# Performance work log

Measured on AMD Instinct MI355X. Metric: run time of the kernel, lower is better.

## Reference

```python
import jax, jax.numpy as jnp
import numpy as np

NUM_CLASSES = 10  # matches label fill_max; original iterates over train_label.unique()


def setup_inputs() -> dict:
    key = jax.random.key(0)
    k1, k2, k3 = jax.random.split(key, 3)
    n, m, d = 8192, 50000, 128
    x = jax.random.normal(k1, (n, d), dtype=jnp.float32)
    train_pts = jax.random.normal(k2, (m, d), dtype=jnp.float32)
    train_label = jax.random.randint(k3, (m,), 0, NUM_CLASSES, dtype=jnp.int32)
    return {"x": x, "train_pts": train_pts, "train_label": train_label, "k": 10}


def reference(x, train_pts, train_label, k):
    # Euclidean distance matrix [n, m]; same math as expand/pow/sum without the
    x2 = jnp.sum(x * x, axis=1, keepdims=True)          # [n, 1]
    y2 = jnp.sum(train_pts * train_pts, axis=1)         # [m]
    sq = x2 + y2[None, :] - 2.0 * (x @ train_pts.T)     # [n, m]
    dist = jnp.sqrt(jnp.maximum(sq, 0.0))
    # k smallest distances -> neighbor indices
    _, idx = jax.lax.top_k(-dist, k)                    # [n, k]
    votes = train_label[idx]                            # [n, k]
    # per-class vote counts; original loop: for lab in sorted unique labels,
    # who = count >= best -> ties go to the LARGEST label
    counts = jnp.sum(jax.nn.one_hot(votes, NUM_CLASSES, dtype=jnp.int32), axis=1)  # [n, C]
    winner = (NUM_CLASSES - 1) - jnp.argmax(counts[:, ::-1], axis=1)
    return winner.astype(train_label.dtype)
```

## Files before the change

### kernel.cpp

```cpp
#include <hip/hip_runtime.h>
#include <float.h>
#include <limits.h>

#define N_Q 8192
#define M_PTS 50000
#define DIM 128
#define KNN 10
#define NCLS 10
#define NCHUNK 16
#define TPC 196
#define CPC 8
#define NCAND (NCHUNK*CPC)
#define NSEL 24
#define TPL 6
#define QPB 128
#define SBIAS 256.0f
#define YTHREADS 200000
#define PTHREADS 232768
#define ATHREADS 232944

typedef __attribute__((ext_vector_type(8))) int i32x8;
typedef __attribute__((ext_vector_type(4))) float f32x4;
typedef unsigned int u32;

__device__ __forceinline__ u32 pack4_e4m3(float4 v, float sc) {
    u32 w = 0;
    w = __builtin_amdgcn_cvt_pk_fp8_f32(sc * v.x, sc * v.y, w, false);
    w = __builtin_amdgcn_cvt_pk_fp8_f32(sc * v.z, sc * v.w, w, true);
    return w;
}

__global__ __launch_bounds__(256) void prep_kernel(
    const float4* __restrict__ x4, const float4* __restrict__ y4,
    u32* __restrict__ xb8, u32* __restrict__ yt8, float* __restrict__ y2) {
    int t = blockIdx.x * 256 + threadIdx.x;
    if (t < YTHREADS) {
        int T = t >> 6, l = t & 63, nr = l & 15, g = l >> 4;
        const float4* src = y4 + ((size_t)(T * 16 + nr) * DIM + g * 32) / 4;
        u32 w[8];
        float ss = 0.f;
        #pragma unroll
        for (int i = 0; i < 8; ++i) {
            float4 v = src[i];
            ss += v.x * v.x + v.y * v.y + v.z * v.z + v.w * v.w;
            w[i] = pack4_e4m3(v, 1.0f);
        }
        uint4* dst = (uint4*)(yt8 + (size_t)T * 512 + l * 8);
        dst[0] = make_uint4(w[0], w[1], w[2], w[3]);
        dst[1] = make_uint4(w[4], w[5], w[6], w[7]);
        ss += __shfl_xor(ss, 16, 64);
        ss += __shfl_xor(ss, 32, 64);
        if (l < 16) y2[T * 16 + l] = ss + SBIAS;
    } else if (t < PTHREADS) {
        int tx = t - YTHREADS, row = tx >> 2, g = tx & 3;
        const float4* src = x4 + ((size_t)row * DIM + g * 32) / 4;
        u32 w[8];
        #pragma unroll
        for (int i = 0; i < 8; ++i) w[i] = pack4_e4m3(src[i], -2.0f);
        uint4* dst = (uint4*)(xb8 + (size_t)row * 32 + g * 8);
        dst[0] = make_uint4(w[0], w[1], w[2], w[3]);
        dst[1] = make_uint4(w[4], w[5], w[6], w[7]);
    } else if (t < ATHREADS) {
        y2[M_PTS + (t - PTHREADS)] = FLT_MAX;
    }
}

__global__ __launch_bounds__(256, 4) void knn_filter(
    const u32* __restrict__ xb8, const u32* __restrict__ yt8,
    const float* __restrict__ y2, u32* __restrict__ ckey) {
    const int lane = threadIdx.x & 63;
    const int wid  = threadIdx.x >> 6;
    const int g    = lane >> 4;
    const int nrow = lane & 15;
    const int chunk = blockIdx.x;
    const int qb    = blockIdx.y;
    const int qw = qb * QPB + wid * 32;

    i32x8 bq0 = *(const i32x8*)(xb8 + (size_t)(qw + nrow) * 32 + g * 8);
    i32x8 bq1 = *(const i32x8*)(xb8 + (size_t)(qw + 16 + nrow) * 32 + g * 8);

    float ts0[TPL], ts1[TPL];
    #pragma unroll
    for (int l = 0; l < TPL; ++l) { ts0[l] = FLT_MAX; ts1[l] = FLT_MAX; }

    const u32* ytp = yt8 + (size_t)chunk * TPC * 512 + lane * 8;
    const f32x4* y2p = (const f32x4*)(y2 + chunk * TPC * 16 + g * 4);

    #pragma unroll 2
    for (int t = 0; t < TPC; ++t) {
        i32x8 ay = *(const i32x8*)(ytp + (size_t)t * 512);
        f32x4 cq = y2p[t * 4];
        f32x4 d0 = __builtin_amdgcn_mfma_scale_f32_16x16x128_f8f6f4(
            ay, bq0, cq, 0, 0, 0, 0x7F7F7F7F, 0, 0x7F7F7F7F);
        f32x4 d1 = __builtin_amdgcn_mfma_scale_f32_16x16x128_f8f6f4(
            ay, bq1, cq, 0, 0, 0, 0x7F7F7F7F, 0, 0x7F7F7F7F);
        u32 relb = (u32)(t * 16) | (u32)(g * 4);
        #pragma unroll
        for (int i = 0; i < 4; ++i) {
            float k0 = __uint_as_float((__float_as_uint(d0[i]) & 0xFFFFF000u) | (relb + i));
            float k1 = __uint_as_float((__float_as_uint(d1[i]) & 0xFFFFF000u) | (relb + i));
            float a0 = ts0[0], a1 = ts0[1], a2 = ts0[2], a3 = ts0[3], a4 = ts0[4];
            float b0 = ts1[0], b1 = ts1[1], b2 = ts1[2], b3 = ts1[3], b4 = ts1[4];
            ts0[0] = fminf(a0, k0);
            ts1[0] = fminf(b0, k1);
            ts0[1] = __builtin_amdgcn_fmed3f(k0, a0, a1);
            ts1[1] = __builtin_amdgcn_fmed3f(k1, b0, b1);
            ts0[2] = __builtin_amdgcn_fmed3f(k0, a1, a2);
            ts1[2] = __builtin_amdgcn_fmed3f(k1, b1, b2);
            ts0[3] = __builtin_amdgcn_fmed3f(k0, a2, a3);
            ts1[3] = __builtin_amdgcn_fmed3f(k1, b2, b3);
            ts0[4] = __builtin_amdgcn_fmed3f(k0, a3, a4);
            ts1[4] = __builtin_amdgcn_fmed3f(k1, b3, b4);
            ts0[5] = __builtin_amdgcn_fmed3f(k0, a4, ts0[5]);
            ts1[5] = __builtin_amdgcn_fmed3f(k1, b4, ts1[5]);
        }
    }

    __shared__ u32 smem[QPB * 25];
    {
        int ql0 = wid * 32 + nrow;
        int ql1 = wid * 32 + 16 + nrow;
        #pragma unroll
        for (int l = 0; l < TPL; ++l) {
            smem[ql0 * 25 + g * TPL + l] = __float_as_uint(ts0[l]);
            smem[ql1 * 25 + g * TPL + l] = __float_as_uint(ts1[l]);
        }
    }
    __syncthreads();
    if (threadIdx.x < QPB) {
        int ql = threadIdx.x;
        float bs[CPC];
        #pragma unroll
        for (int i = 0; i < CPC; ++i) bs[i] = FLT_MAX;
        for (int e = 0; e < 4 * TPL; ++e) {
            float f = __uint_as_float(smem[ql * 25 + e]);
            #pragma unroll
            for (int q2 = 0; q2 < CPC; ++q2) {
                float mn = fminf(bs[q2], f);
                f = fmaxf(bs[q2], f);
                bs[q2] = mn;
            }
        }
        u32* dst = ckey + ((size_t)(qb * QPB + ql) * NCHUNK + chunk) * CPC;
        #pragma unroll
        for (int i = 0; i < CPC; ++i) dst[i] = __float_as_uint(bs[i]);
    }
}

__global__ __launch_bounds__(256) void knn_finalize(
    const u32* __restrict__ ckey, const float* __restrict__ x,
    const float* __restrict__ y, const int* __restrict__ labels,
    int* __restrict__ out) {
    const int lane = threadIdx.x & 63;
    const int wid  = threadIdx.x >> 6;
    const int qbase = blockIdx.x * 8;
    const int ql = wid * 2 + (lane >> 5);
    const int sl = lane & 31;

    __shared__ u32 skey[8][NCAND];
    __shared__ int sidx[8][NSEL];
    __shared__ double sex[8][NSEL];

    for (int i = threadIdx.x; i < 8 * NCAND; i += 256)
        skey[i >> 7][i & 127] = ckey[(size_t)(qbase + (i >> 7)) * NCAND + (i & 127)];
    __syncthreads();

    {
        u32 ke[4];
        int rank[4];
        #pragma unroll
        for (int r0 = 0; r0 < 4; ++r0) {
            ke[r0] = skey[ql][r0 * 32 + sl];
            rank[r0] = 0;
        }
        for (int j = 0; j < NCAND; ++j) {
            u32 kj = skey[ql][j];
            #pragma unroll
            for (int r0 = 0; r0 < 4; ++r0)
                rank[r0] += (kj < ke[r0] || (kj == ke[r0] && j < r0 * 32 + sl)) ? 1 : 0;
        }
        #pragma unroll
        for (int r0 = 0; r0 < 4; ++r0) {
            if (rank[r0] < NSEL) {
                int e = r0 * 32 + sl;
                sidx[ql][rank[r0]] = (e >> 3) * (TPC * 16) + (int)(ke[r0] & 0xFFFu);
            }
        }
    }
    __syncthreads();

    if (sl < NSEL) {
        const int idx = sidx[ql][sl];
        const float4* xr = (const float4*)(x + (size_t)(qbase + ql) * DIM);
        const float4* yr = (const float4*)(y + (size_t)idx * DIM);
        double dy2 = 0.0, dxy = 0.0;
        #pragma unroll 8
        for (int i = 0; i < 32; ++i) {
            float4 yv = yr[i];
            float4 xv = xr[i];
            dy2 = fma((double)yv.x, (double)yv.x, dy2);
            dy2 = fma((double)yv.y, (double)yv.y, dy2);
            dy2 = fma((double)yv.z, (double)yv.z, dy2);
            dy2 = fma((double)yv.w, (double)yv.w, dy2);
            dxy = fma((double)xv.x, (double)yv.x, dxy);
            dxy = fma((double)xv.y, (double)yv.y, dxy);
            dxy = fma((double)xv.z, (double)yv.z, dxy);
            dxy = fma((double)xv.w, (double)yv.w, dxy);
        }
        sex[ql][sl] = dy2 - 2.0 * dxy;
    }
    __syncthreads();

    if (sl == 0) {
        double tsv[KNN]; int ti[KNN];
        #pragma unroll
        for (int i = 0; i < KNN; ++i) { tsv[i] = 1e300; ti[i] = INT_MAX; }
        #pragma unroll
        for (int c = 0; c < NSEL; ++c) {
            double s = sex[ql][c];
            int id = sidx[ql][c];
            #pragma unroll
            for (int pp = 0; pp < KNN; ++pp) {
                bool lt = (s < tsv[pp]) || (s == tsv[pp] && id < ti[pp]);
                double ns = lt ? tsv[pp] : s;  int nid = lt ? ti[pp] : id;
                tsv[pp] = lt ? s : tsv[pp];    ti[pp] = lt ? id : ti[pp];
                s = ns; id = nid;
            }
        }
        int lab[KNN];
        #pragma unroll
        for (int i = 0; i < KNN; ++i) lab[i] = labels[ti[i]];
        int bestc = 0, bestn = -1;
        #pragma unroll
        for (int c = 0; c < NCLS; ++c) {
            int n = 0;
            #pragma unroll
            for (int i = 0; i < KNN; ++i) n += (lab[i] == c) ? 1 : 0;
            if (n >= bestn) { bestn = n; bestc = c; }
        }
        out[qbase + ql] = bestc;
    }
}

extern "C" void kernel_launch(void* const* d_in, const int* in_sizes, int n_in,
                              void* d_out, int out_size, void* d_ws, size_t ws_size,
                              hipStream_t stream) {
    const float* x      = (const float*)d_in[0];
    const float* y      = (const float*)d_in[1];
    const int*   labels = (const int*)d_in[2];

    char* ws = (char*)d_ws;
    size_t off = 0;
    u32* xb8 = (u32*)(ws + off);    off += (size_t)N_Q * DIM;
    u32* yt8 = (u32*)(ws + off);    off += (size_t)NCHUNK * TPC * 2048;
    float* y2 = (float*)(ws + off); off += (size_t)NCHUNK * TPC * 16 * 4;
    u32* ckey = (u32*)(ws + off);   off += (size_t)N_Q * NCAND * 4;
    int* out = (int*)d_out;

    prep_kernel<<<(ATHREADS + 255) / 256, 256, 0, stream>>>(
        (const float4*)x, (const float4*)y, xb8, yt8, y2);
    knn_filter<<<dim3(NCHUNK, N_Q / QPB), 256, 0, stream>>>(xb8, yt8, y2, ckey);
    knn_finalize<<<N_Q / 8, 256, 0, stream>>>(ckey, x, y, labels, out);
}
```

Measured before the change: 274.0 us.

## Prefetch tiles in filter loop and coalesce prep with one float4 per thread

The filter kernel's main loop now loads the next pair of FP8 tiles and their norm vectors before running the MFMA and top-k updates on the current pair. This is register double-buffering meant to hide global load latency behind compute. The prep kernel is rewritten so each thread converts one float4, which makes the fp32 reads coalesced. Row norms are then reduced with a 32-lane shuffle tree, at the cost of scattered 4-byte stores into the tiled layout. The prefetch also raises register pressure under launch bounds of (256,4).

```diff
diff --git a/kernel.cpp b/kernel.cpp
--- a/kernel.cpp
+++ b/kernel.cpp
@@ -15,9 +15,8 @@
 #define TPL 6
 #define QPB 128
 #define SBIAS 256.0f
-#define YTHREADS 200000
-#define PTHREADS 232768
-#define ATHREADS 232944
+#define XN4 (N_Q*DIM/4)
+#define YN4 (M_PTS*DIM/4)
 
 typedef __attribute__((ext_vector_type(8))) int i32x8;
 typedef __attribute__((ext_vector_type(4))) float f32x4;
@@ -34,34 +33,23 @@
     const float4* __restrict__ x4, const float4* __restrict__ y4,
     u32* __restrict__ xb8, u32* __restrict__ yt8, float* __restrict__ y2) {
     int t = blockIdx.x * 256 + threadIdx.x;
-    if (t < YTHREADS) {
-        int T = t >> 6, l = t & 63, nr = l & 15, g = l >> 4;
-        const float4* src = y4 + ((size_t)(T * 16 + nr) * DIM + g * 32) / 4;
-        u32 w[8];
-        float ss = 0.f;
-        #pragma unroll
-        for (int i = 0; i < 8; ++i) {
-            float4 v = src[i];
-            ss += v.x * v.x + v.y * v.y + v.z * v.z + v.w * v.w;
-            w[i] = pack4_e4m3(v, 1.0f);
-        }
-        uint4* dst = (uint4*)(yt8 + (size_t)T * 512 + l * 8);
-        dst[0] = make_uint4(w[0], w[1], w[2], w[3]);
-        dst[1] = make_uint4(w[4], w[5], w[6], w[7]);
-        ss += __shfl_xor(ss, 16, 64);
-        ss += __shfl_xor(ss, 32, 64);
-        if (l < 16) y2[T * 16 + l] = ss + SBIAS;
-    } else if (t < PTHREADS) {
-        int tx = t - YTHREADS, row = tx >> 2, g = tx & 3;
-        const float4* src = x4 + ((size_t)row * DIM + g * 32) / 4;
-        u32 w[8];
-        #pragma unroll
-        for (int i = 0; i < 8; ++i) w[i] = pack4_e4m3(src[i], -2.0f);
-        uint4* dst = (uint4*)(xb8 + (size_t)row * 32 + g * 8);
-        dst[0] = make_uint4(w[0], w[1], w[2], w[3]);
-        dst[1] = make_uint4(w[4], w[5], w[6], w[7]);
-    } else if (t < ATHREADS) {
-        y2[M_PTS + (t - PTHREADS)] = FLT_MAX;
+    if (t < XN4) {
+        xb8[t] = pack4_e4m3(x4[t], -2.0f);
+    } else if (t < XN4 + YN4) {
+        int j = t - XN4;
+        int row = j >> 5;
+        int d4  = j & 31;
+        float4 v = y4[j];
+        u32 w = pack4_e4m3(v, 1.0f);
+        int T = row >> 4, nr = row & 15;
+        int g2 = d4 >> 3, s = d4 & 7;
+        yt8[(size_t)T * 512 + (g2 * 16 + nr) * 8 + s] = w;
+        float p = v.x * v.x + v.y * v.y + v.z * v.z + v.w * v.w;
+        #pragma unroll
+        for (int off = 16; off > 0; off >>= 1) p += __shfl_xor(p, off, 64);
+        if (d4 == 0) y2[row] = p + SBIAS;
+    } else if (t < XN4 + YN4 + 176) {
+        y2[M_PTS + (t - XN4 - YN4)] = FLT_MAX;
     }
 }
 
@@ -86,10 +74,7 @@
     const u32* ytp = yt8 + (size_t)chunk * TPC * 512 + lane * 8;
     const f32x4* y2p = (const f32x4*)(y2 + chunk * TPC * 16 + g * 4);
 
-    #pragma unroll 2
-    for (int t = 0; t < TPC; ++t) {
-        i32x8 ay = *(const i32x8*)(ytp + (size_t)t * 512);
-        f32x4 cq = y2p[t * 4];
+    auto process = [&](i32x8 ay, f32x4 cq, int t) {
         f32x4 d0 = __builtin_amdgcn_mfma_scale_f32_16x16x128_f8f6f4(
             ay, bq0, cq, 0, 0, 0, 0x7F7F7F7F, 0, 0x7F7F7F7F);
         f32x4 d1 = __builtin_amdgcn_mfma_scale_f32_16x16x128_f8f6f4(
@@ -114,7 +99,26 @@
             ts0[5] = __builtin_amdgcn_fmed3f(k0, a4, ts0[5]);
             ts1[5] = __builtin_amdgcn_fmed3f(k1, b4, ts1[5]);
         }
-    }
+    };
+
+    i32x8 ayA = *(const i32x8*)(ytp);
+    i32x8 ayB = *(const i32x8*)(ytp + 512);
+    f32x4 cqA = y2p[0];
+    f32x4 cqB = y2p[4];
+
+    int t = 0;
+    for (; t < TPC - 2; t += 2) {
+        i32x8 nA = *(const i32x8*)(ytp + (size_t)(t + 2) * 512);
+        f32x4 pA = y2p[(t + 2) * 4];
+        process(ayA, cqA, t);
+        ayA = nA; cqA = pA;
+        i32x8 nB = *(const i32x8*)(ytp + (size_t)(t + 3) * 512);
+        f32x4 pB = y2p[(t + 3) * 4];
+        process(ayB, cqB, t + 1);
+        ayB = nB; cqB = pB;
+    }
+    process(ayA, cqA, TPC - 2);
+    process(ayB, cqB, TPC - 1);
 
     __shared__ u32 smem[QPB * 25];
     {
@@ -257,7 +261,7 @@
     u32* ckey = (u32*)(ws + off);   off += (size_t)N_Q * NCAND * 4;
     int* out = (int*)d_out;
 
-    prep_kernel<<<(ATHREADS + 255) / 256, 256, 0, stream>>>(
+    prep_kernel<<<(XN4 + YN4 + 176 + 255) / 256, 256, 0, stream>>>(
         (const float4*)x, (const float4*)y, xb8, yt8, y2);
     knn_filter<<<dim3(NCHUNK, N_Q / QPB), 256, 0, stream>>>(xb8, yt8, y2, ckey);
     knn_finalize<<<N_Q / 8, 256, 0, stream>>>(ckey, x, y, labels, out);
```

Result: faster. 268.2 us (-2.1%).
